# Kernel tuning notes

Measured on AMD Instinct MI355X. Metric: run time of the kernel, lower is better.

The kernel has to match this reference:

```python
import jax, jax.numpy as jnp
import numpy as np

B, C, D, H, W = 4, 128, 16, 16, 16
INNER = 64  # channels // reduction


def setup_inputs() -> dict:
    key = jax.random.key(0)
    ks = jax.random.split(key, 4)
    s = 0.02
    return {
        "x": jax.random.normal(ks[0], (B, C, D, H, W), dtype=jnp.float32),
        "Wq": jax.random.normal(ks[1], (INNER, C), dtype=jnp.float32) * s,
        "bq": jnp.zeros((INNER,), dtype=jnp.float32),
        "Wk": jax.random.normal(ks[2], (INNER, C), dtype=jnp.float32) * s,
        "bk": jnp.zeros((INNER,), dtype=jnp.float32),
        "Wv": jax.random.normal(ks[3], (C, C), dtype=jnp.float32) * s,
        "bv": jnp.zeros((C,), dtype=jnp.float32),
        "gamma": jnp.zeros((1,), dtype=jnp.float32),
    }


def reference(x, Wq, bq, Wk, bk, Wv, bv, gamma):
    b, c, d, h, w = x.shape
    n = d * h * w
    inner = Wq.shape[0]
    scale = inner ** (-0.5)
    xf = x.reshape(b, c, n)  # flatten spatial dims
    # 1x1 Conv3d == per-position channel matmul
    q = jnp.einsum('oc,bcn->bon', Wq, xf) + bq[None, :, None]  # [B, inner, N]
    k = jnp.einsum('oc,bcn->bon', Wk, xf) + bk[None, :, None]  # [B, inner, N]
    v = jnp.einsum('oc,bcn->bon', Wv, xf) + bv[None, :, None]  # [B, C, N]
    # attn[b, n, m] = softmax_m(q[:, :, n] . k[:, :, m] * scale)
    attn = jax.nn.softmax(jnp.einsum('bon,bom->bnm', q, k) * scale, axis=-1)
    # out = v @ attn^T  -> out[b, c, n] = sum_m v[b, c, m] * attn[b, n, m]
    out = jnp.einsum('bcm,bnm->bcn', v, attn).reshape(b, c, d, h, w)
    return x + gamma[0] * out
```

## Files before the change

kernel.cpp:

```cpp
#include <hip/hip_runtime.h>
#include <cstdint>

#define B_ 4
#define C_ 128
#define INNER_ 64
#define N_ 4096
#define SPLITS 8
#define KT 32
#define NTS 16

typedef __attribute__((ext_vector_type(8))) short short8;
typedef __attribute__((ext_vector_type(4))) short bf16x4;
typedef __attribute__((ext_vector_type(4))) float f32x4;
typedef __attribute__((ext_vector_type(2))) unsigned u32x2;
typedef __attribute__((ext_vector_type(4))) unsigned u32x4;

typedef const __attribute__((address_space(1))) void* gp_t;
typedef __attribute__((address_space(3))) void* lp_t;

#define WAITBAR3() asm volatile("s_waitcnt vmcnt(3)\n\ts_barrier" ::: "memory")
#define WAITBAR0() asm volatile("s_waitcnt vmcnt(0)\n\ts_barrier" ::: "memory")

__device__ __forceinline__ short f2bf(float f) {
  unsigned u = __builtin_bit_cast(unsigned, f);
  unsigned r = (u + 0x7FFFu + ((u >> 16) & 1u)) >> 16;
  return (short)r;
}
__device__ __forceinline__ float bf2f(short s) {
  return __builtin_bit_cast(float, ((unsigned)(unsigned short)s) << 16);
}
__device__ __forceinline__ float fexp2(float x) {
#if __has_builtin(__builtin_amdgcn_exp2f)
  return __builtin_amdgcn_exp2f(x);
#else
  return exp2f(x);
#endif
}
__device__ __forceinline__ unsigned pk2(float lo, float hi) {
#if __has_builtin(__builtin_amdgcn_cvt_pk_bf16_f32)
  typedef __attribute__((ext_vector_type(2))) __bf16 bfp;
  bfp v = __builtin_amdgcn_cvt_pk_bf16_f32(lo, hi);
  return __builtin_bit_cast(unsigned, v);
#else
  return (unsigned)(unsigned short)f2bf(lo) | ((unsigned)(unsigned short)f2bf(hi) << 16);
#endif
}

__global__ __launch_bounds__(256) void pack_kernel(
    const float* __restrict__ Wq, const float* __restrict__ bq,
    const float* __restrict__ Wk, const float* __restrict__ bk,
    const float* __restrict__ Wv, const float* __restrict__ bv,
    short* __restrict__ wp, float* __restrict__ bp)
{
  const int idx = blockIdx.x * 256 + threadIdx.x;
  const int o = idx >> 7, c = idx & 127;
  float v;
  if (o < 64)       v = Wq[o * C_ + c];
  else if (o < 128) v = Wk[(o - 64) * C_ + c];
  else              v = Wv[(o - 128) * C_ + c];
  wp[idx] = f2bf(v);
  if (c == 0)
    bp[o] = (o < 64) ? bq[o] : (o < 128) ? bk[o - 64] : bv[o - 128];
}

__global__ __launch_bounds__(256) void qkv_kernel(
    const float* __restrict__ x, const short* __restrict__ wp,
    const float* __restrict__ bp,
    short* __restrict__ qg, short* __restrict__ kg, short* __restrict__ vg)
{
  __shared__ short xT[32 * 136];
  __shared__ short outb[256 * 40];
  __shared__ float biasL[256];

  const int tid = threadIdx.x;
  const int b   = blockIdx.x >> 7;
  const int n0  = (blockIdx.x & 127) << 5;
  const float QSC = 0.125f * 1.44269504088896340736f;

  biasL[tid] = bp[tid];
  const float* xb = x + (size_t)b * C_ * N_ + n0;
  for (int i = tid; i < 1024; i += 256) {
    const int c = i >> 3, seg = i & 7;
    const float4 v = *(const float4*)&xb[(size_t)c * N_ + seg * 4];
    xT[(seg * 4 + 0) * 136 + c] = f2bf(v.x);
    xT[(seg * 4 + 1) * 136 + c] = f2bf(v.y);
    xT[(seg * 4 + 2) * 136 + c] = f2bf(v.z);
    xT[(seg * 4 + 3) * 136 + c] = f2bf(v.w);
  }
  __syncthreads();

  const int w = tid >> 6, lane = tid & 63, quad = lane >> 4, l16 = lane & 15;

  short8 xf[2][4];
#pragma unroll
  for (int nt = 0; nt < 2; ++nt)
#pragma unroll
    for (int kk = 0; kk < 4; ++kk)
      xf[nt][kk] = *(const short8*)&xT[(nt * 16 + l16) * 136 + kk * 32 + quad * 8];

  if (w < 2) {
    const int obase = w * 64;
    const float osc = (w == 0) ? QSC : 1.0f;
#pragma unroll
    for (int ot = 0; ot < 4; ++ot) {
      const int o = obase + ot * 16 + l16;
      short8 wf[4];
#pragma unroll
      for (int kk = 0; kk < 4; ++kk)
        wf[kk] = *(const short8*)&wp[(size_t)o * 128 + kk * 32 + quad * 8];
      const float bias = biasL[o];
#pragma unroll
      for (int nt = 0; nt < 2; ++nt) {
        f32x4 acc = (f32x4){0.f, 0.f, 0.f, 0.f};
#pragma unroll
        for (int kk = 0; kk < 4; ++kk)
          acc = __builtin_amdgcn_mfma_f32_16x16x32_bf16(xf[nt][kk], wf[kk], acc, 0, 0, 0);
#pragma unroll
        for (int r = 0; r < 4; ++r)
          outb[o * 40 + nt * 16 + quad * 4 + r] = f2bf((acc[r] + bias) * osc);
      }
    }
  } else {
    const int ob2 = (w - 2) * 64;
#pragma unroll
    for (int ot = 0; ot < 4; ++ot) {
      const int orow = 128 + ob2 + ot * 16 + l16;
      short8 wf[4];
#pragma unroll
      for (int kk = 0; kk < 4; ++kk)
        wf[kk] = *(const short8*)&wp[(size_t)orow * 128 + kk * 32 + quad * 8];
#pragma unroll
      for (int nt = 0; nt < 2; ++nt) {
        f32x4 acc = (f32x4){0.f, 0.f, 0.f, 0.f};
#pragma unroll
        for (int kk = 0; kk < 4; ++kk)
          acc = __builtin_amdgcn_mfma_f32_16x16x32_bf16(wf[kk], xf[nt][kk], acc, 0, 0, 0);
#pragma unroll
        for (int r = 0; r < 4; ++r) {
          const int o_r = 128 + ob2 + ot * 16 + quad * 4 + r;
          outb[o_r * 40 + nt * 16 + l16] = f2bf(acc[r] + biasL[o_r]);
        }
      }
    }
  }
  __syncthreads();

  {
    const int n = tid >> 3, oc = tid & 7;
    short8 qv, kv;
#pragma unroll
    for (int j = 0; j < 8; ++j) {
      qv[j] = outb[(oc * 8 + j) * 40 + n];
      kv[j] = outb[(64 + oc * 8 + j) * 40 + n];
    }
    *(short8*)&qg[(((size_t)b * N_ + n0 + n) << 6) + oc * 8] = qv;
    *(short8*)&kg[(((size_t)b * N_ + n0 + n) << 6) + oc * 8] = kv;
  }
  {
    const int T = n0 >> 5;
#pragma unroll
    for (int rep = 0; rep < 2; ++rep) {
      const int idx2 = rep * 256 + tid;
      const int ch = idx2 >> 2, q = idx2 & 3;
      const bf16x4 lo = *(const bf16x4*)&outb[(128 + ch) * 40 + q * 4];
      const bf16x4 hi = *(const bf16x4*)&outb[(128 + ch) * 40 + 16 + q * 4];
      short8 vv;
#pragma unroll
      for (int j = 0; j < 4; ++j) { vv[j] = lo[j]; vv[4 + j] = hi[j]; }
      const size_t tb = ((size_t)b * 128 + T) * 4096 + (size_t)idx2 * 8;
      *(short8*)&vg[tb] = vv;
    }
  }
}

__global__ __launch_bounds__(256, 2) void attn_kernel(
    const short* __restrict__ qb, const short* __restrict__ kb,
    const short* __restrict__ vb,
    short* __restrict__ Opart, float* __restrict__ lbuf)
{
  __shared__ short kbuf[3][2048];
  __shared__ short vbuf[3][4096];

  const int tid = threadIdx.x;
  const int bid = blockIdx.x;
  const int s   = bid & 7;
  const int qg  = (bid >> 3) & 15;
  const int b   = bid >> 7;
  const int m0  = qg << 8;
  const int w   = tid >> 6, lane = tid & 63, quad = lane >> 4, l16 = lane & 15;
  const int rbase = m0 + w * 64;

  short8 qa[4][2];
#pragma unroll
  for (int mt = 0; mt < 4; ++mt)
#pragma unroll
    for (int kk = 0; kk < 2; ++kk)
      qa[mt][kk] = *(const short8*)&qb[((size_t)b * N_ + rbase + mt * 16 + l16) * 64 + kk * 32 + quad * 8];

  float lsum[4] = {0.f, 0.f, 0.f, 0.f};
  f32x4 accO[8][4];
#pragma unroll
  for (int vt = 0; vt < 8; ++vt)
#pragma unroll
    for (int mt = 0; mt < 4; ++mt) accO[vt][mt] = (f32x4){0.f, 0.f, 0.f, 0.f};

  auto dma_tile = [&](int kt, int d) {
    const int T = s * NTS + kt;
    const short* kbp = kb + (((size_t)b * N_ + T * 32) << 6);
    {
      const int p = w * 64 + lane;
      const int key = p >> 3, jm = (p & 7) ^ (key & 7);
      __builtin_amdgcn_global_load_lds((gp_t)(kbp + (key << 6) + jm * 8),
                                       (lp_t)&kbuf[d][w * 512], 16, 0, 0);
    }
    const short* vtp = vb + ((size_t)b * 128 + T) * 4096;
#pragma unroll
    for (int t = 0; t < 2; ++t) {
      const int p = (w * 2 + t) * 64 + lane;
      __builtin_amdgcn_global_load_lds((gp_t)(vtp + p * 8),
                                       (lp_t)&vbuf[d][(w * 2 + t) * 512], 16, 0, 0);
    }
  };

  dma_tile(0, 0);
  dma_tile(1, 1);

#pragma unroll
  for (int kt = 0; kt < NTS; ++kt) {
    if (kt + 1 < NTS) { WAITBAR3(); } else { WAITBAR0(); }
    if (kt + 2 < NTS) dma_tile(kt + 2, (kt + 2) % 3);
    const int d = kt % 3;

    u32x2 ppk[2][4];
#pragma unroll
    for (int ct = 0; ct < 2; ++ct) {
      const short8 kf0 = *(const short8*)&kbuf[d][((ct * 16 + l16) << 6) + ((quad ^ (l16 & 7)) << 3)];
      const short8 kf1 = *(const short8*)&kbuf[d][((ct * 16 + l16) << 6) + (((4 + quad) ^ (l16 & 7)) << 3)];
#pragma unroll
      for (int mt = 0; mt < 4; ++mt) {
        f32x4 st = (f32x4){0.f, 0.f, 0.f, 0.f};
        st = __builtin_amdgcn_mfma_f32_16x16x32_bf16(kf0, qa[mt][0], st, 0, 0, 0);
        st = __builtin_amdgcn_mfma_f32_16x16x32_bf16(kf1, qa[mt][1], st, 0, 0, 0);
        const float p0 = fexp2(st[0]);
        const float p1 = fexp2(st[1]);
        const float p2 = fexp2(st[2]);
        const float p3 = fexp2(st[3]);
        lsum[mt] += (p0 + p1) + (p2 + p3);
        u32x2 pp;
        pp[0] = pk2(p0, p1);
        pp[1] = pk2(p2, p3);
        ppk[ct][mt] = pp;
      }
    }
    short8 pcat[4];
#pragma unroll
    for (int mt = 0; mt < 4; ++mt) {
      u32x4 u = (u32x4){ppk[0][mt][0], ppk[0][mt][1], ppk[1][mt][0], ppk[1][mt][1]};
      pcat[mt] = __builtin_bit_cast(short8, u);
    }

#pragma unroll
    for (int vt = 0; vt < 8; ++vt) {
      const short8 vf = *(const short8*)&vbuf[d][((vt * 16 + l16) << 5) + (quad << 3)];
#pragma unroll
      for (int mt = 0; mt < 4; ++mt)
        accO[vt][mt] = __builtin_amdgcn_mfma_f32_16x16x32_bf16(vf, pcat[mt], accO[vt][mt], 0, 0, 0);
    }
  }

#pragma unroll
  for (int mt = 0; mt < 4; ++mt) {
    lsum[mt] += __shfl_xor(lsum[mt], 16);
    lsum[mt] += __shfl_xor(lsum[mt], 32);
  }
  if (quad == 0) {
#pragma unroll
    for (int mt = 0; mt < 4; ++mt)
      lbuf[((size_t)b * SPLITS + s) * N_ + rbase + mt * 16 + l16] = lsum[mt];
  }
#pragma unroll
  for (int vt = 0; vt < 8; ++vt) {
#pragma unroll
    for (int mt = 0; mt < 4; ++mt) {
#pragma unroll
      for (int r = 0; r < 4; ++r) {
        const int ch = vt * 16 + quad * 4 + r;
        Opart[(((size_t)b * SPLITS + s) * C_ + ch) * N_ + rbase + mt * 16 + l16] =
            f2bf(accO[vt][mt][r]);
      }
    }
  }
}

__global__ __launch_bounds__(256) void combine_kernel(
    const float* __restrict__ x, const float* __restrict__ gamma,
    const short* __restrict__ Opart, const float* __restrict__ lbuf,
    float* __restrict__ out)
{
  __shared__ float linvL[64];
  const int tid = threadIdx.x;
  const int b   = blockIdx.x >> 6;
  const int n0  = (blockIdx.x & 63) << 6;

  if (tid < 64) {
    float L = 0.f;
#pragma unroll
    for (int s = 0; s < SPLITS; ++s) L += lbuf[((size_t)b * SPLITS + s) * N_ + n0 + tid];
    linvL[tid] = 1.f / L;
  }
  __syncthreads();

  const float g = gamma[0];
  const int n4 = (tid & 15) * 4, cb = tid >> 4;
#pragma unroll
  for (int cp = 0; cp < 8; ++cp) {
    const int c = cp * 16 + cb;
    float acc[4] = {0.f, 0.f, 0.f, 0.f};
#pragma unroll
    for (int s = 0; s < SPLITS; ++s) {
      const bf16x4 o4 = *(const bf16x4*)&Opart[(((size_t)b * SPLITS + s) * C_ + c) * N_ + n0 + n4];
#pragma unroll
      for (int j = 0; j < 4; ++j) acc[j] += bf2f(o4[j]);
    }
    const size_t xi = ((size_t)b * C_ + c) * N_ + n0 + n4;
    const float4 xv = *(const float4*)&x[xi];
    float4 ov;
    ov.x = xv.x + g * acc[0] * linvL[n4 + 0];
    ov.y = xv.y + g * acc[1] * linvL[n4 + 1];
    ov.z = xv.z + g * acc[2] * linvL[n4 + 2];
    ov.w = xv.w + g * acc[3] * linvL[n4 + 3];
    *(float4*)&out[xi] = ov;
  }
}

extern "C" void kernel_launch(void* const* d_in, const int* in_sizes, int n_in,
                              void* d_out, int out_size, void* d_ws, size_t ws_size,
                              hipStream_t stream) {
  const float* x     = (const float*)d_in[0];
  const float* Wq    = (const float*)d_in[1];
  const float* bq    = (const float*)d_in[2];
  const float* Wk    = (const float*)d_in[3];
  const float* bk    = (const float*)d_in[4];
  const float* Wv    = (const float*)d_in[5];
  const float* bv    = (const float*)d_in[6];
  const float* gamma = (const float*)d_in[7];
  float* out = (float*)d_out;

  short* qb = (short*)d_ws;
  short* kb = qb + (size_t)B_ * N_ * INNER_;
  short* vb = kb + (size_t)B_ * N_ * INNER_;
  short* Opart = vb + (size_t)B_ * C_ * N_;
  float* lbuf  = (float*)(Opart + (size_t)B_ * SPLITS * C_ * N_);
  float* bp    = lbuf + (size_t)B_ * SPLITS * N_;
  short* wp    = (short*)(bp + 256);

  pack_kernel<<<128, 256, 0, stream>>>(Wq, bq, Wk, bk, Wv, bv, wp, bp);
  qkv_kernel<<<B_ * (N_ / 32), 256, 0, stream>>>(x, wp, bp, qb, kb, vb);
  attn_kernel<<<B_ * 16 * SPLITS, 256, 0, stream>>>(qb, kb, vb, Opart, lbuf);
  combine_kernel<<<B_ * (N_ / 64), 256, 0, stream>>>(x, gamma, Opart, lbuf, out);
}
```

Baseline: 123.4 us.

## Switch attention to single-wave blocks with fewer KV splits and no barriers

```diff
diff --git a/kernel.cpp b/kernel.cpp
--- a/kernel.cpp
+++ b/kernel.cpp
@@ -5,9 +5,9 @@
 #define C_ 128
 #define INNER_ 64
 #define N_ 4096
-#define SPLITS 8
+#define SPLITS 4
 #define KT 32
-#define NTS 16
+#define NTS 32
 
 typedef __attribute__((ext_vector_type(8))) short short8;
 typedef __attribute__((ext_vector_type(4))) short bf16x4;
@@ -18,8 +18,8 @@
 typedef const __attribute__((address_space(1))) void* gp_t;
 typedef __attribute__((address_space(3))) void* lp_t;
 
-#define WAITBAR3() asm volatile("s_waitcnt vmcnt(3)\n\ts_barrier" ::: "memory")
-#define WAITBAR0() asm volatile("s_waitcnt vmcnt(0)\n\ts_barrier" ::: "memory")
+#define WAITCNT12() asm volatile("s_waitcnt vmcnt(12)" ::: "memory")
+#define WAITCNT0()  asm volatile("s_waitcnt vmcnt(0)"  ::: "memory")
 
 __device__ __forceinline__ short f2bf(float f) {
   unsigned u = __builtin_bit_cast(unsigned, f);
@@ -173,7 +173,7 @@
   }
 }
 
-__global__ __launch_bounds__(256, 2) void attn_kernel(
+__global__ __launch_bounds__(64) void attn_kernel(
     const short* __restrict__ qb, const short* __restrict__ kb,
     const short* __restrict__ vb,
     short* __restrict__ Opart, float* __restrict__ lbuf)
@@ -183,12 +183,11 @@
 
   const int tid = threadIdx.x;
   const int bid = blockIdx.x;
-  const int s   = bid & 7;
-  const int qg  = (bid >> 3) & 15;
-  const int b   = bid >> 7;
-  const int m0  = qg << 8;
-  const int w   = tid >> 6, lane = tid & 63, quad = lane >> 4, l16 = lane & 15;
-  const int rbase = m0 + w * 64;
+  const int s   = bid & 3;
+  const int qgr = (bid >> 2) & 63;
+  const int b   = bid >> 8;
+  const int lane = tid & 63, quad = lane >> 4, l16 = lane & 15;
+  const int rbase = qgr << 6;
 
   short8 qa[4][2];
 #pragma unroll
@@ -207,18 +206,18 @@
   auto dma_tile = [&](int kt, int d) {
     const int T = s * NTS + kt;
     const short* kbp = kb + (((size_t)b * N_ + T * 32) << 6);
-    {
-      const int p = w * 64 + lane;
+#pragma unroll
+    for (int t = 0; t < 4; ++t) {
+      const int p = t * 64 + lane;
       const int key = p >> 3, jm = (p & 7) ^ (key & 7);
       __builtin_amdgcn_global_load_lds((gp_t)(kbp + (key << 6) + jm * 8),
-                                       (lp_t)&kbuf[d][w * 512], 16, 0, 0);
+                                       (lp_t)&kbuf[d][t * 512], 16, 0, 0);
     }
     const short* vtp = vb + ((size_t)b * 128 + T) * 4096;
 #pragma unroll
-    for (int t = 0; t < 2; ++t) {
-      const int p = (w * 2 + t) * 64 + lane;
-      __builtin_amdgcn_global_load_lds((gp_t)(vtp + p * 8),
-                                       (lp_t)&vbuf[d][(w * 2 + t) * 512], 16, 0, 0);
+    for (int t = 0; t < 8; ++t) {
+      __builtin_amdgcn_global_load_lds((gp_t)(vtp + (t * 64 + lane) * 8),
+                                       (lp_t)&vbuf[d][t * 512], 16, 0, 0);
     }
   };
 
@@ -227,15 +226,17 @@
 
 #pragma unroll
   for (int kt = 0; kt < NTS; ++kt) {
-    if (kt + 1 < NTS) { WAITBAR3(); } else { WAITBAR0(); }
+    if (kt + 1 < NTS) { WAITCNT12(); } else { WAITCNT0(); }
     if (kt + 2 < NTS) dma_tile(kt + 2, (kt + 2) % 3);
     const int d = kt % 3;
+    const short* kh = kbuf[d];
+    const short* vh = vbuf[d];
 
     u32x2 ppk[2][4];
 #pragma unroll
     for (int ct = 0; ct < 2; ++ct) {
-      const short8 kf0 = *(const short8*)&kbuf[d][((ct * 16 + l16) << 6) + ((quad ^ (l16 & 7)) << 3)];
-      const short8 kf1 = *(const short8*)&kbuf[d][((ct * 16 + l16) << 6) + (((4 + quad) ^ (l16 & 7)) << 3)];
+      const short8 kf0 = *(const short8*)&kh[((ct * 16 + l16) << 6) + ((quad ^ (l16 & 7)) << 3)];
+      const short8 kf1 = *(const short8*)&kh[((ct * 16 + l16) << 6) + (((4 + quad) ^ (l16 & 7)) << 3)];
 #pragma unroll
       for (int mt = 0; mt < 4; ++mt) {
         f32x4 st = (f32x4){0.f, 0.f, 0.f, 0.f};
@@ -261,7 +262,7 @@
 
 #pragma unroll
     for (int vt = 0; vt < 8; ++vt) {
-      const short8 vf = *(const short8*)&vbuf[d][((vt * 16 + l16) << 5) + (quad << 3)];
+      const short8 vf = *(const short8*)&vh[((vt * 16 + l16) << 5) + (quad << 3)];
 #pragma unroll
       for (int mt = 0; mt < 4; ++mt)
         accO[vt][mt] = __builtin_amdgcn_mfma_f32_16x16x32_bf16(vf, pcat[mt], accO[vt][mt], 0, 0, 0);
@@ -356,6 +357,6 @@
 
   pack_kernel<<<128, 256, 0, stream>>>(Wq, bq, Wk, bk, Wv, bv, wp, bp);
   qkv_kernel<<<B_ * (N_ / 32), 256, 0, stream>>>(x, wp, bp, qb, kb, vb);
-  attn_kernel<<<B_ * 16 * SPLITS, 256, 0, stream>>>(qb, kb, vb, Opart, lbuf);
+  attn_kernel<<<B_ * 64 * SPLITS, 64, 0, stream>>>(qb, kb, vb, Opart, lbuf);
   combine_kernel<<<B_ * (N_ / 64), 256, 0, stream>>>(x, gamma, Opart, lbuf, out);
 }
```

After: 213.7 us. 73.2% more time.
